# Performance work log

Hardware: AMD Instinct MI355X
Metric: run time of the kernel (lower is better)

## Reference

```python
import jax, jax.numpy as jnp
import numpy as np

B, N, D, H, L = 16, 1024, 256, 128, 2  # batch, nodes, feat dim, gcn_hidden, n_layers (D == 2*H)


def setup_inputs() -> dict:
    key = jax.random.key(0)
    ks = jax.random.split(key, 16)
    inp = {
        "gcn_input": jax.random.normal(ks[0], (B, N, D), jnp.float32),
        # scale adjacencies by 1/N so aggregated features stay O(1)
        "latent_adj": jax.random.uniform(ks[1], (B, N, N), jnp.float32) / N,
        "dep_adj": jax.random.uniform(ks[2], (B, N, N), jnp.float32) / N,
        # stacked per-layer parameters (leading dim L); layers share shapes since D == 2*H
        "refine_gate": jax.random.normal(ks[3], (L, D, 1), jnp.float32) * 0.02,
        "gate_W_in": jax.random.normal(ks[4], (L, D, 1), jnp.float32) * 0.02,
        "gate_b_in": jnp.zeros((L, 1), jnp.float32),
        "gate_W_out": jax.random.normal(ks[5], (L, D, 1), jnp.float32) * 0.02,
        "gate_b_out": jnp.zeros((L, 1), jnp.float32),
        "fc_in_W": jax.random.normal(ks[6], (L, H, D), jnp.float32) * 0.02,
        "fc_in_b": jnp.zeros((L, H), jnp.float32),
        "fc_out_W": jax.random.normal(ks[7], (L, H, D), jnp.float32) * 0.02,
        "fc_out_b": jnp.zeros((L, H), jnp.float32),
        "ln_g": jnp.ones((L, 2 * H), jnp.float32),
        "ln_b": jnp.zeros((L, 2 * H), jnp.float32),
    }
    return inp


def _gcn_layer(x, latent, dep, rg, Wgi, bgi, Wgo, bgo, Wi, bi, Wo, bo, g, b):
    # refine gate blends dependency and latent adjacency per source node
    gate = jax.nn.sigmoid(x @ rg)  # [B,N,1]
    A_in = gate * dep + (1.0 - gate) * latent  # [B,N,N]
    A_out = gate * jnp.swapaxes(dep, -1, -2) + (1.0 - gate) * jnp.swapaxes(latent, -1, -2)
    Ax_in = A_in @ x   # [B,N,D]
    Ax_out = A_out @ x
    # gcn gates (scalar bias added after the gated product, as in torch)
    Ax_in = Ax_in * jax.nn.sigmoid(Ax_in @ Wgi) + bgi
    Ax_out = Ax_out * jax.nn.sigmoid(Ax_out @ Wgo) + bgo
    # rec_fc(Ax) + rec_fc(x): weight applied to sum, bias counted twice (faithful)
    h_in = (Ax_in + x) @ Wi.T + 2.0 * bi   # [B,N,H]
    h_out = (Ax_out + x) @ Wo.T + 2.0 * bo
    h = jnp.concatenate([h_in, h_out], axis=-1)  # [B,N,2H]
    mu = jnp.mean(h, axis=-1, keepdims=True)
    var = jnp.var(h, axis=-1, keepdims=True)
    h = (h - mu) * jax.lax.rsqrt(var + 1e-5) * g + b
    return jax.nn.gelu(h, approximate=False)


def reference(gcn_input, latent_adj, dep_adj, refine_gate, gate_W_in, gate_b_in,
              gate_W_out, gate_b_out, fc_in_W, fc_in_b, fc_out_W, fc_out_b, ln_g, ln_b):
    x = gcn_input
    for l in range(refine_gate.shape[0]):  # small fixed layer count
        x = _gcn_layer(x, latent_adj, dep_adj, refine_gate[l],
                       gate_W_in[l], gate_b_in[l], gate_W_out[l], gate_b_out[l],
                       fc_in_W[l], fc_in_b[l], fc_out_W[l], fc_out_b[l],
                       ln_g[l], ln_b[l])
    return x
```

## Files before the change

### kernel.cpp

```cpp
#include <hip/hip_runtime.h>
#include <hip/hip_bf16.h>
#include <cstdint>

#define B_ 16
#define N_ 1024
#define D_ 256
#define H_ 128

typedef unsigned short u16;
typedef __attribute__((ext_vector_type(8))) short bf16x8;
typedef __attribute__((ext_vector_type(4))) float f32x4;

__device__ __forceinline__ u16 f2bf(float f) {
    union { float f; uint32_t u; } v; v.f = f;
    return (u16)((v.u + 0x7FFFu + ((v.u >> 16) & 1u)) >> 16);
}

typedef __attribute__((address_space(3))) void lds_void;
typedef const __attribute__((address_space(1))) void g_void;

__device__ __forceinline__ void gl_lds16(const void* g, void* l) {
    __builtin_amdgcn_global_load_lds((g_void*)g, (lds_void*)l, 16, 0, 0);
}

__device__ __forceinline__ void vm_wait5() { asm volatile("s_waitcnt vmcnt(5)" ::: "memory"); }
__device__ __forceinline__ void vm_wait0() { asm volatile("s_waitcnt vmcnt(0)" ::: "memory"); }

__global__ __launch_bounds__(256) void k_conv_adj(
    const float* __restrict__ dep, const float* __restrict__ lat,
    u16* __restrict__ depb, u16* __restrict__ latb,
    u16* __restrict__ depTb, u16* __restrict__ latTb)
{
    __shared__ u16 tile[64][64];
    const int bz = blockIdx.z;
    const int b = bz >> 1;
    const float* src = (bz & 1) ? lat : dep;
    u16* dstN = (bz & 1) ? latb : depb;
    u16* dstT = (bz & 1) ? latTb : depTb;
    const int r0 = blockIdx.y * 64, c0 = blockIdx.x * 64;
    const int t = threadIdx.x;
    const int r = t >> 2, cg = (t & 3) * 16;

    const float* srow = src + ((size_t)b * N_ + r0 + r) * N_ + c0 + cg;
    bf16x8 lo, hi;
    {
        const float4 v0 = *(const float4*)(srow);
        const float4 v1 = *(const float4*)(srow + 4);
        const float4 v2 = *(const float4*)(srow + 8);
        const float4 v3 = *(const float4*)(srow + 12);
        lo[0] = (short)f2bf(v0.x); lo[1] = (short)f2bf(v0.y); lo[2] = (short)f2bf(v0.z); lo[3] = (short)f2bf(v0.w);
        lo[4] = (short)f2bf(v1.x); lo[5] = (short)f2bf(v1.y); lo[6] = (short)f2bf(v1.z); lo[7] = (short)f2bf(v1.w);
        hi[0] = (short)f2bf(v2.x); hi[1] = (short)f2bf(v2.y); hi[2] = (short)f2bf(v2.z); hi[3] = (short)f2bf(v2.w);
        hi[4] = (short)f2bf(v3.x); hi[5] = (short)f2bf(v3.y); hi[6] = (short)f2bf(v3.z); hi[7] = (short)f2bf(v3.w);
    }
    u16* nrow = dstN + ((size_t)b * N_ + r0 + r) * N_ + c0 + cg;
    *(bf16x8*)nrow = lo;
    *(bf16x8*)(nrow + 8) = hi;

    const int g0 = (t & 3) * 2;
    const int s = r & 7;
    *(bf16x8*)(&tile[r][((g0    ) ^ s) * 8]) = lo;
    *(bf16x8*)(&tile[r][((g0 + 1) ^ s) * 8]) = hi;
    __syncthreads();

    const int sc = t >> 2, rg2 = (t & 3) * 16;
    bf16x8 o0, o1;
    #pragma unroll
    for (int i = 0; i < 8; ++i) {
        const int R = rg2 + i;
        o0[i] = (short)tile[R][(((sc >> 3) ^ (R & 7)) * 8) + (sc & 7)];
    }
    #pragma unroll
    for (int i = 0; i < 8; ++i) {
        const int R = rg2 + 8 + i;
        o1[i] = (short)tile[R][(((sc >> 3) ^ (R & 7)) * 8) + (sc & 7)];
    }
    u16* dT = dstT + ((size_t)b * N_ + c0 + sc) * N_ + r0 + rg2;
    *(bf16x8*)dT = o0;
    *(bf16x8*)(dT + 8) = o1;
}

__global__ __launch_bounds__(256) void k_gate_xt(
    const float* __restrict__ x, const float* __restrict__ rg,
    float* __restrict__ gate, u16* __restrict__ xT,
    const float* __restrict__ wi, const float* __restrict__ wo,
    u16* __restrict__ wib, u16* __restrict__ wob)
{
    if (blockIdx.y >= B_) {
        const int i = ((blockIdx.y - B_) * 32 + blockIdx.x) * 256 + threadIdx.x;
        wib[i] = f2bf(wi[i]);
        wob[i] = f2bf(wo[i]);
        return;
    }

    __shared__ u16 lx[D_][36];
    __shared__ float srg[D_];
    const int b = blockIdx.y, n0 = blockIdx.x * 32;
    const int t = threadIdx.x;
    srg[t] = rg[t];
    __syncthreads();

    const int r = t >> 3, cg = t & 7;
    const float* xrow = x + ((size_t)b * N_ + n0 + r) * D_;
    float dot = 0.f;
    #pragma unroll
    for (int u = 0; u < 8; ++u) {
        const int c = cg * 32 + u * 4;
        const float4 v = *(const float4*)(xrow + c);
        lx[c][r] = f2bf(v.x); lx[c + 1][r] = f2bf(v.y);
        lx[c + 2][r] = f2bf(v.z); lx[c + 3][r] = f2bf(v.w);
        dot += v.x * srg[c] + v.y * srg[c + 1] + v.z * srg[c + 2] + v.w * srg[c + 3];
    }
    dot += __shfl_down(dot, 4, 8);
    dot += __shfl_down(dot, 2, 8);
    dot += __shfl_down(dot, 1, 8);
    if (cg == 0) gate[(size_t)b * N_ + n0 + r] = 1.f / (1.f + expf(-dot));
    __syncthreads();

    #pragma unroll
    for (int i = 0; i < 8; ++i) {
        const int unit = i * 256 + t;
        const int d = unit >> 3, nch = (unit & 7) * 4;
        ushort4 wv;
        wv.x = lx[d][nch];     wv.y = lx[d][nch + 1];
        wv.z = lx[d][nch + 2]; wv.w = lx[d][nch + 3];
        *(ushort4*)(xT + ((size_t)b * D_ + d) * N_ + n0 + nch) = wv;
    }
}

__global__ __launch_bounds__(256, 2) void k_gemm_ax(
    const u16* __restrict__ depb, const u16* __restrict__ latb,
    const u16* __restrict__ depTb, const u16* __restrict__ latTb,
    const u16* __restrict__ xT,
    const float* __restrict__ gate,
    const float* __restrict__ Wgi, const float* __restrict__ Wgo,
    const float* __restrict__ bgi, const float* __restrict__ bgo,
    const float* __restrict__ xcur,
    u16* __restrict__ axin, u16* __restrict__ axout)
{
    __shared__ __align__(16) char smem[61696];
    float* hbuf = (float*)smem;
    float* sh_g = (float*)(smem + 61440);
    float* sh_s = (float*)(smem + 61568);

    const int bid = blockIdx.x;
    const int logical = (bid & 7) * 128 + (bid >> 3);
    const int b = logical >> 6;
    const int rem = logical & 63;
    const int z = rem >> 5;
    const int m0 = (rem & 31) * 32;

    const u16* A1 = z ? depTb : depb;
    const u16* A2 = z ? latTb : latb;
    const float* Wg = z ? Wgo : Wgi;
    const float bg0 = z ? bgo[0] : bgi[0];
    u16* outp = z ? axout : axin;

    const int t = threadIdx.x;
    const int lane = t & 63;
    const int w = t >> 6;

    f32x4 acc1[2][4], acc2[2][4];
    const f32x4 fz = {0.f, 0.f, 0.f, 0.f};
    #pragma unroll
    for (int i = 0; i < 2; ++i)
        #pragma unroll
        for (int j = 0; j < 4; ++j) { acc1[i][j] = fz; acc2[i][j] = fz; }

    const u16* gsrc[5];
    int loff[5];
    const int rl = lane >> 2;
    const int kk = (((lane & 3) ^ ((lane >> 3) & 3)) << 3);
    #pragma unroll
    for (int ci = 0; ci < 5; ++ci) {
        const int c = w * 5 + ci;
        if (c < 4) {
            const int cc = c & 1;
            const int m = cc * 16 + rl;
            const u16* base = (c < 2) ? A1 : A2;
            gsrc[ci] = base + ((size_t)b * N_ + m0 + m) * N_ + kk;
            loff[ci] = ((c < 2) ? 0 : 1024) + cc * 512;
        } else {
            const int cc = c - 4;
            const int n = cc * 16 + rl;
            gsrc[ci] = xT + ((size_t)b * D_ + n) * N_ + kk;
            loff[ci] = 2048 + cc * 512;
        }
    }

    u16* const sb = (u16*)smem;

    #pragma unroll
    for (int ci = 0; ci < 5; ++ci) gl_lds16(gsrc[ci], sb + loff[ci]);
    #pragma unroll
    for (int ci = 0; ci < 5; ++ci) { gl_lds16(gsrc[ci] + 32, sb + 10240 + loff[ci]); gsrc[ci] += 64; }

    const int mrow = lane & 15;
    const int kg = (((lane >> 4) ^ ((mrow >> 1) & 3)) << 3);

    for (int ks = 0; ks < N_ / 32; ++ks) {
        if (ks == 31) vm_wait0(); else vm_wait5();
        __builtin_amdgcn_s_barrier();
        __builtin_amdgcn_sched_barrier(0);
        if (ks <= 29) {
            u16* nb = sb + ((ks + 2) % 3) * 10240;
            #pragma unroll
            for (int ci = 0; ci < 5; ++ci) { gl_lds16(gsrc[ci], nb + loff[ci]); gsrc[ci] += 32; }
        }
        const u16* cur = sb + (ks % 3) * 10240;
        const u16* sA1 = cur;
        const u16* sA2 = cur + 1024;
        const u16* sB  = cur + 2048;
        bf16x8 a1[2], a2[2], fb[4];
        #pragma unroll
        for (int mt = 0; mt < 2; ++mt) {
            const int row = mt * 16 + mrow;
            a1[mt] = *(const bf16x8*)(sA1 + row * 32 + kg);
            a2[mt] = *(const bf16x8*)(sA2 + row * 32 + kg);
        }
        #pragma unroll
        for (int nt = 0; nt < 4; ++nt) {
            const int row = w * 64 + nt * 16 + mrow;
            fb[nt] = *(const bf16x8*)(sB + row * 32 + kg);
        }
        #pragma unroll
        for (int mt = 0; mt < 2; ++mt)
            #pragma unroll
            for (int nt = 0; nt < 4; ++nt) {
                acc1[mt][nt] = __builtin_amdgcn_mfma_f32_16x16x32_bf16(a1[mt], fb[nt], acc1[mt][nt], 0, 0, 0);
                acc2[mt][nt] = __builtin_amdgcn_mfma_f32_16x16x32_bf16(a2[mt], fb[nt], acc2[mt][nt], 0, 0, 0);
            }
    }
    __syncthreads();

    if (t < 32) sh_g[t] = gate[(size_t)b * N_ + m0 + t];
    __syncthreads();

    const int hi = lane >> 4;
    #pragma unroll
    for (int mt = 0; mt < 2; ++mt)
        #pragma unroll
        for (int nt = 0; nt < 4; ++nt) {
            const int col = w * 64 + nt * 16 + mrow;
            #pragma unroll
            for (int rr = 0; rr < 4; ++rr) {
                const int row = mt * 16 + hi * 4 + rr;
                const float g = sh_g[row];
                hbuf[row * 260 + col] = g * acc1[mt][nt][rr] + (1.f - g) * acc2[mt][nt][rr];
            }
        }
    __syncthreads();

    {
        const int rr = t >> 3;
        const int c0 = (t & 7) * 32;
        float dot = 0.f;
        #pragma unroll 8
        for (int u = 0; u < 32; ++u) dot += hbuf[rr * 260 + c0 + u] * Wg[c0 + u];
        dot += __shfl_down(dot, 4, 8);
        dot += __shfl_down(dot, 2, 8);
        dot += __shfl_down(dot, 1, 8);
        if ((t & 7) == 0) sh_s[rr] = 1.f / (1.f + expf(-dot));
    }
    __syncthreads();

    #pragma unroll
    for (int i = 0; i < 16; ++i) {
        const int row = (t >> 7) + i * 2;
        const int c = (t & 127) * 2;
        const float s = sh_s[row];
        const size_t gidx = ((size_t)b * N_ + m0 + row) * D_ + c;
        const float2 xv = *(const float2*)(xcur + gidx);
        const float v0 = hbuf[row * 260 + c] * s + bg0 + xv.x;
        const float v1 = hbuf[row * 260 + c + 1] * s + bg0 + xv.y;
        *(ushort2*)(outp + gidx) = make_ushort2(f2bf(v0), f2bf(v1));
    }
}

__global__ __launch_bounds__(256, 2) void k_fc_ln(
    const u16* __restrict__ axin, const u16* __restrict__ axout,
    const u16* __restrict__ Wib, const u16* __restrict__ Wob,
    const float* __restrict__ bi, const float* __restrict__ bo,
    const float* __restrict__ lg, const float* __restrict__ lb,
    float* __restrict__ outp)
{
    __shared__ __align__(16) char smem[61696];
    float* hbuf = (float*)smem;
    float* sh_mu = (float*)(smem + 61440);
    float* sh_rs = (float*)(smem + 61568);

    const int b = blockIdx.y, m0 = blockIdx.x * 32;
    const int t = threadIdx.x, lane = t & 63, w = t >> 6;
    const int half = w >> 1, wn = w & 1;

    f32x4 acc[2][4];
    const f32x4 fz = {0.f, 0.f, 0.f, 0.f};
    #pragma unroll
    for (int i = 0; i < 2; ++i)
        #pragma unroll
        for (int j = 0; j < 4; ++j) acc[i][j] = fz;

    const u16* gsrc[5];
    int loff[5];
    const int rl = lane >> 2;
    const int kk = (((lane & 3) ^ ((lane >> 3) & 3)) << 3);
    #pragma unroll
    for (int ci = 0; ci < 5; ++ci) {
        const int c = w * 5 + ci;
        if (c < 4) {
            const int cc = c & 1;
            const int m = cc * 16 + rl;
            const u16* base = (c < 2) ? axin : axout;
            gsrc[ci] = base + ((size_t)b * N_ + m0 + m) * D_ + kk;
            loff[ci] = ((c < 2) ? 0 : 1024) + cc * 512;
        } else {
            const int cc = (c - 4) & 7;
            const int n = cc * 16 + rl;
            const u16* base = (c < 12) ? Wib : Wob;
            gsrc[ci] = base + (size_t)n * D_ + kk;
            loff[ci] = ((c < 12) ? 2048 : 6144) + cc * 512;
        }
    }

    u16* const sb = (u16*)smem;

    #pragma unroll
    for (int ci = 0; ci < 5; ++ci) gl_lds16(gsrc[ci], sb + loff[ci]);
    #pragma unroll
    for (int ci = 0; ci < 5; ++ci) { gl_lds16(gsrc[ci] + 32, sb + 10240 + loff[ci]); gsrc[ci] += 64; }

    const int mrow = lane & 15;
    const int kg = (((lane >> 4) ^ ((mrow >> 1) & 3)) << 3);

    for (int ks = 0; ks < D_ / 32; ++ks) {
        if (ks == 7) vm_wait0(); else vm_wait5();
        __builtin_amdgcn_s_barrier();
        __builtin_amdgcn_sched_barrier(0);
        if (ks <= 5) {
            u16* nb = sb + ((ks + 2) % 3) * 10240;
            #pragma unroll
            for (int ci = 0; ci < 5; ++ci) { gl_lds16(gsrc[ci], nb + loff[ci]); gsrc[ci] += 32; }
        }
        const u16* cur = sb + (ks % 3) * 10240;
        const u16* sA = cur + (half ? 1024 : 0);
        const u16* sW = cur + 2048 + (half ? 4096 : 0);
        bf16x8 a[2], fb[4];
        #pragma unroll
        for (int mt = 0; mt < 2; ++mt)
            a[mt] = *(const bf16x8*)(sA + (mt * 16 + mrow) * 32 + kg);
        #pragma unroll
        for (int nt = 0; nt < 4; ++nt)
            fb[nt] = *(const bf16x8*)(sW + (wn * 64 + nt * 16 + mrow) * 32 + kg);
        #pragma unroll
        for (int mt = 0; mt < 2; ++mt)
            #pragma unroll
            for (int nt = 0; nt < 4; ++nt)
                acc[mt][nt] = __builtin_amdgcn_mfma_f32_16x16x32_bf16(a[mt], fb[nt], acc[mt][nt], 0, 0, 0);
    }
    __syncthreads();

    const int hi = lane >> 4;
    #pragma unroll
    for (int mt = 0; mt < 2; ++mt)
        #pragma unroll
        for (int nt = 0; nt < 4; ++nt) {
            const int colh = wn * 64 + nt * 16 + mrow;
            const int col = half * 128 + colh;
            const float bias = 2.f * (half ? bo[colh] : bi[colh]);
            #pragma unroll
            for (int rr = 0; rr < 4; ++rr) {
                const int row = mt * 16 + hi * 4 + rr;
                hbuf[row * 260 + col] = acc[mt][nt][rr] + bias;
            }
        }
    __syncthreads();

    {
        const int rr = t >> 3;
        const int c0 = (t & 7) * 32;
        float s = 0.f, ss = 0.f;
        #pragma unroll 8
        for (int u = 0; u < 32; ++u) {
            const float v = hbuf[rr * 260 + c0 + u];
            s += v; ss += v * v;
        }
        s += __shfl_down(s, 4, 8);  ss += __shfl_down(ss, 4, 8);
        s += __shfl_down(s, 2, 8);  ss += __shfl_down(ss, 2, 8);
        s += __shfl_down(s, 1, 8);  ss += __shfl_down(ss, 1, 8);
        if ((t & 7) == 0) {
            const float mu = s * (1.f / 256.f);
            const float var = ss * (1.f / 256.f) - mu * mu;
            sh_mu[rr] = mu;
            sh_rs[rr] = rsqrtf(var + 1e-5f);
        }
    }
    __syncthreads();

    #pragma unroll
    for (int i = 0; i < 16; ++i) {
        const int row = (t >> 7) + i * 2;
        const int c = (t & 127) * 2;
        const float mu = sh_mu[row], rs = sh_rs[row];
        const float2 gg = *(const float2*)(lg + c);
        const float2 bb = *(const float2*)(lb + c);
        const float v0 = (hbuf[row * 260 + c] - mu) * rs * gg.x + bb.x;
        const float v1 = (hbuf[row * 260 + c + 1] - mu) * rs * gg.y + bb.y;
        const float y0 = 0.5f * v0 * (1.f + erff(v0 * 0.70710678118654752f));
        const float y1 = 0.5f * v1 * (1.f + erff(v1 * 0.70710678118654752f));
        const size_t gidx = ((size_t)b * N_ + m0 + row) * D_ + c;
        *(float2*)(outp + gidx) = make_float2(y0, y1);
    }
}

extern "C" void kernel_launch(void* const* d_in, const int* in_sizes, int n_in,
                              void* d_out, int out_size, void* d_ws, size_t ws_size,
                              hipStream_t stream)
{
    (void)in_sizes; (void)n_in; (void)out_size; (void)ws_size;

    const float* x0  = (const float*)d_in[0];
    const float* lat = (const float*)d_in[1];
    const float* dep = (const float*)d_in[2];
    const float* rg  = (const float*)d_in[3];
    const float* Wgi = (const float*)d_in[4];
    const float* bgi = (const float*)d_in[5];
    const float* Wgo = (const float*)d_in[6];
    const float* bgo = (const float*)d_in[7];
    const float* fiW = (const float*)d_in[8];
    const float* fib = (const float*)d_in[9];
    const float* foW = (const float*)d_in[10];
    const float* fob = (const float*)d_in[11];
    const float* lng = (const float*)d_in[12];
    const float* lnb = (const float*)d_in[13];

    char* ws = (char*)d_ws;
    size_t off = 0;
    auto alloc = [&](size_t bytes) {
        char* p = ws + off;
        off += (bytes + 255) & ~(size_t)255;
        return p;
    };
    u16* depb  = (u16*)alloc(2ull * B_ * N_ * N_);
    u16* latb  = (u16*)alloc(2ull * B_ * N_ * N_);
    u16* depTb = (u16*)alloc(2ull * B_ * N_ * N_);
    u16* latTb = (u16*)alloc(2ull * B_ * N_ * N_);
    u16* xT    = (u16*)alloc(2ull * B_ * D_ * N_);
    u16* axin  = (u16*)alloc(2ull * B_ * N_ * D_);
    u16* axout = (u16*)alloc(2ull * B_ * N_ * D_);
    float* gate = (float*)alloc(4ull * B_ * N_);
    float* xbuf = (float*)alloc(4ull * B_ * N_ * D_);
    u16* Wib = (u16*)alloc(2ull * H_ * D_);
    u16* Wob = (u16*)alloc(2ull * H_ * D_);

    k_conv_adj<<<dim3(16, 16, 32), 256, 0, stream>>>(dep, lat, depb, latb, depTb, latTb);

    const float* xcur = x0;
    for (int l = 0; l < 2; ++l) {
        k_gate_xt<<<dim3(32, B_ + 4), 256, 0, stream>>>(
            xcur, rg + l * D_, gate, xT,
            fiW + (size_t)l * H_ * D_, foW + (size_t)l * H_ * D_, Wib, Wob);
        k_gemm_ax<<<dim3(1024), 256, 0, stream>>>(
            depb, latb, depTb, latTb, xT, gate,
            Wgi + l * D_, Wgo + l * D_, bgi + l, bgo + l,
            xcur, axin, axout);
        const bool last = (l == 1);
        k_fc_ln<<<dim3(32, B_), 256, 0, stream>>>(
            axin, axout, Wib, Wob,
            fib + l * H_, fob + l * H_,
            lng + l * 2 * H_, lnb + l * 2 * H_,
            last ? (float*)d_out : xbuf);
        xcur = xbuf;
    }
}
```

Measured before the change: 352.6 us.

## Blend adjacencies before the GEMM and enlarge aggregation tiles to 128 rows

```diff
diff --git a/kernel.cpp b/kernel.cpp
--- a/kernel.cpp
+++ b/kernel.cpp
@@ -15,6 +15,10 @@
     union { float f; uint32_t u; } v; v.f = f;
     return (u16)((v.u + 0x7FFFu + ((v.u >> 16) & 1u)) >> 16);
 }
+__device__ __forceinline__ float bf2f(u16 h) {
+    union { uint32_t u; float f; } v; v.u = ((uint32_t)h) << 16;
+    return v.f;
+}
 
 typedef __attribute__((address_space(3))) void lds_void;
 typedef const __attribute__((address_space(1))) void g_void;
@@ -23,8 +27,10 @@
     __builtin_amdgcn_global_load_lds((g_void*)g, (lds_void*)l, 16, 0, 0);
 }
 
-__device__ __forceinline__ void vm_wait5() { asm volatile("s_waitcnt vmcnt(5)" ::: "memory"); }
+__device__ __forceinline__ void vm_wait4() { asm volatile("s_waitcnt vmcnt(4)" ::: "memory"); }
+__device__ __forceinline__ void vm_wait2() { asm volatile("s_waitcnt vmcnt(2)" ::: "memory"); }
 __device__ __forceinline__ void vm_wait0() { asm volatile("s_waitcnt vmcnt(0)" ::: "memory"); }
+__device__ __forceinline__ void lgkm0()   { asm volatile("s_waitcnt lgkmcnt(0)" ::: "memory"); }
 
 __global__ __launch_bounds__(256) void k_conv_adj(
     const float* __restrict__ dep, const float* __restrict__ lat,
@@ -128,7 +134,7 @@
     }
 }
 
-__global__ __launch_bounds__(256, 2) void k_gemm_ax(
+__global__ __launch_bounds__(512, 2) void k_gemm_ax(
     const u16* __restrict__ depb, const u16* __restrict__ latb,
     const u16* __restrict__ depTb, const u16* __restrict__ latTb,
     const u16* __restrict__ xT,
@@ -138,17 +144,18 @@
     const float* __restrict__ xcur,
     u16* __restrict__ axin, u16* __restrict__ axout)
 {
-    __shared__ __align__(16) char smem[61696];
+    __shared__ __align__(16) char smem[51712];
+    u16* const sb = (u16*)smem;
     float* hbuf = (float*)smem;
-    float* sh_g = (float*)(smem + 61440);
-    float* sh_s = (float*)(smem + 61568);
+    float* psum = (float*)(smem + 49152);
+    float* sh_s = (float*)(smem + 51200);
 
     const int bid = blockIdx.x;
-    const int logical = (bid & 7) * 128 + (bid >> 3);
-    const int b = logical >> 6;
-    const int rem = logical & 63;
-    const int z = rem >> 5;
-    const int m0 = (rem & 31) * 32;
+    const int logical = (bid & 7) * 32 + (bid >> 3);
+    const int b = logical >> 4;
+    const int rem = logical & 15;
+    const int z = rem >> 3;
+    const int m0 = (rem & 7) * 128;
 
     const u16* A1 = z ? depTb : depb;
     const u16* A2 = z ? latTb : latb;
@@ -159,121 +166,162 @@
     const int t = threadIdx.x;
     const int lane = t & 63;
     const int w = t >> 6;
-
-    f32x4 acc1[2][4], acc2[2][4];
-    const f32x4 fz = {0.f, 0.f, 0.f, 0.f};
-    #pragma unroll
-    for (int i = 0; i < 2; ++i)
-        #pragma unroll
-        for (int j = 0; j < 4; ++j) { acc1[i][j] = fz; acc2[i][j] = fz; }
-
-    const u16* gsrc[5];
-    int loff[5];
+    const int wr = w >> 2, wc = w & 3;
+
+    const int arow = t >> 2;
+    const int akq = t & 3;
+    const float gv = gate[(size_t)b * N_ + m0 + arow];
+    const u16* gA1 = A1 + ((size_t)b * N_ + m0 + arow) * N_ + akq * 8;
+    const u16* gA2 = A2 + ((size_t)b * N_ + m0 + arow) * N_ + akq * 8;
+    const int awoff = arow * 32 + ((akq ^ ((arow >> 1) & 3)) << 3);
+
     const int rl = lane >> 2;
     const int kk = (((lane & 3) ^ ((lane >> 3) & 3)) << 3);
-    #pragma unroll
-    for (int ci = 0; ci < 5; ++ci) {
-        const int c = w * 5 + ci;
-        if (c < 4) {
-            const int cc = c & 1;
-            const int m = cc * 16 + rl;
-            const u16* base = (c < 2) ? A1 : A2;
-            gsrc[ci] = base + ((size_t)b * N_ + m0 + m) * N_ + kk;
-            loff[ci] = ((c < 2) ? 0 : 1024) + cc * 512;
-        } else {
-            const int cc = c - 4;
-            const int n = cc * 16 + rl;
-            gsrc[ci] = xT + ((size_t)b * D_ + n) * N_ + kk;
-            loff[ci] = 2048 + cc * 512;
-        }
-    }
-
-    u16* const sb = (u16*)smem;
-
-    #pragma unroll
-    for (int ci = 0; ci < 5; ++ci) gl_lds16(gsrc[ci], sb + loff[ci]);
-    #pragma unroll
-    for (int ci = 0; ci < 5; ++ci) { gl_lds16(gsrc[ci] + 32, sb + 10240 + loff[ci]); gsrc[ci] += 64; }
+    const u16* gB0 = xT + ((size_t)b * D_ + (w * 2) * 16 + rl) * N_ + kk;
+    const u16* gB1 = xT + ((size_t)b * D_ + (w * 2 + 1) * 16 + rl) * N_ + kk;
+    const int boff0 = 4096 + (w * 2) * 512;
+    const int boff1 = 4096 + (w * 2 + 1) * 512;
 
     const int mrow = lane & 15;
+    const int hi = lane >> 4;
     const int kg = (((lane >> 4) ^ ((mrow >> 1) & 3)) << 3);
 
-    for (int ks = 0; ks < N_ / 32; ++ks) {
-        if (ks == 31) vm_wait0(); else vm_wait5();
+    f32x4 acc[4][4];
+    const f32x4 fz = {0.f, 0.f, 0.f, 0.f};
+    #pragma unroll
+    for (int i = 0; i < 4; ++i)
+        #pragma unroll
+        for (int j = 0; j < 4; ++j) acc[i][j] = fz;
+
+    bf16x8 rA1x, rA2x, rA1y, rA2y;
+
+    auto blend_store = [&](const bf16x8& a1v, const bf16x8& a2v, u16* dst) {
+        bf16x8 bl;
+        #pragma unroll
+        for (int u = 0; u < 8; ++u) {
+            const float f1 = bf2f((u16)a1v[u]);
+            const float f2 = bf2f((u16)a2v[u]);
+            bl[u] = (short)f2bf(f2 + gv * (f1 - f2));
+        }
+        *(bf16x8*)dst = bl;
+    };
+
+    rA1x = *(const bf16x8*)(gA1);       rA2x = *(const bf16x8*)(gA2);
+    blend_store(rA1x, rA2x, sb + awoff);
+    rA1x = *(const bf16x8*)(gA1 + 32);  rA2x = *(const bf16x8*)(gA2 + 32);
+    gl_lds16(gB0, sb + boff0);          gl_lds16(gB1, sb + boff1);
+    blend_store(rA1x, rA2x, sb + 12288 + awoff);
+    rA1x = *(const bf16x8*)(gA1 + 64);  rA2x = *(const bf16x8*)(gA2 + 64);
+    gl_lds16(gB0 + 32, sb + 12288 + boff0); gl_lds16(gB1 + 32, sb + 12288 + boff1);
+    vm_wait4();
+    lgkm0();
+    __builtin_amdgcn_sched_barrier(0);
+    __builtin_amdgcn_s_barrier();
+    __builtin_amdgcn_sched_barrier(0);
+
+    auto body = [&](int ks, bf16x8& c1, bf16x8& c2, bf16x8& n1, bf16x8& n2) {
+        if (ks <= 28) {
+            n1 = *(const bf16x8*)(gA1 + (ks + 3) * 32);
+            n2 = *(const bf16x8*)(gA2 + (ks + 3) * 32);
+        }
+        const u16* sA = sb + (ks & 1) * 12288;
+        const u16* sBc = sA + 4096;
+        bf16x8 a[4], fbv[4];
+        #pragma unroll
+        for (int mt = 0; mt < 4; ++mt)
+            a[mt] = *(const bf16x8*)(sA + (wr * 64 + mt * 16 + mrow) * 32 + kg);
+        #pragma unroll
+        for (int nt = 0; nt < 4; ++nt)
+            fbv[nt] = *(const bf16x8*)(sBc + (wc * 64 + nt * 16 + mrow) * 32 + kg);
+        #pragma unroll
+        for (int mt = 0; mt < 4; ++mt)
+            #pragma unroll
+            for (int nt = 0; nt < 4; ++nt)
+                acc[mt][nt] = __builtin_amdgcn_mfma_f32_16x16x32_bf16(a[mt], fbv[nt], acc[mt][nt], 0, 0, 0);
+        __builtin_amdgcn_sched_barrier(0);
         __builtin_amdgcn_s_barrier();
         __builtin_amdgcn_sched_barrier(0);
         if (ks <= 29) {
-            u16* nb = sb + ((ks + 2) % 3) * 10240;
-            #pragma unroll
-            for (int ci = 0; ci < 5; ++ci) { gl_lds16(gsrc[ci], nb + loff[ci]); gsrc[ci] += 32; }
-        }
-        const u16* cur = sb + (ks % 3) * 10240;
-        const u16* sA1 = cur;
-        const u16* sA2 = cur + 1024;
-        const u16* sB  = cur + 2048;
-        bf16x8 a1[2], a2[2], fb[4];
-        #pragma unroll
-        for (int mt = 0; mt < 2; ++mt) {
-            const int row = mt * 16 + mrow;
-            a1[mt] = *(const bf16x8*)(sA1 + row * 32 + kg);
-            a2[mt] = *(const bf16x8*)(sA2 + row * 32 + kg);
-        }
-        #pragma unroll
-        for (int nt = 0; nt < 4; ++nt) {
-            const int row = w * 64 + nt * 16 + mrow;
-            fb[nt] = *(const bf16x8*)(sB + row * 32 + kg);
-        }
-        #pragma unroll
-        for (int mt = 0; mt < 2; ++mt)
-            #pragma unroll
-            for (int nt = 0; nt < 4; ++nt) {
-                acc1[mt][nt] = __builtin_amdgcn_mfma_f32_16x16x32_bf16(a1[mt], fb[nt], acc1[mt][nt], 0, 0, 0);
-                acc2[mt][nt] = __builtin_amdgcn_mfma_f32_16x16x32_bf16(a2[mt], fb[nt], acc2[mt][nt], 0, 0, 0);
+            u16* cb = sb + (ks & 1) * 12288;
+            blend_store(c1, c2, cb + awoff);
+            gl_lds16(gB0 + (ks + 2) * 32, cb + boff0);
+            gl_lds16(gB1 + (ks + 2) * 32, cb + boff1);
+        }
+        if (ks <= 28) vm_wait4();
+        else if (ks == 29) vm_wait2();
+        else if (ks == 30) vm_wait0();
+        lgkm0();
+        __builtin_amdgcn_sched_barrier(0);
+        __builtin_amdgcn_s_barrier();
+        __builtin_amdgcn_sched_barrier(0);
+    };
+
+    for (int kp = 0; kp < 16; ++kp) {
+        body(2 * kp,     rA1x, rA2x, rA1y, rA2y);
+        body(2 * kp + 1, rA1y, rA2y, rA1x, rA2x);
+    }
+    __syncthreads();
+
+    float wgv[4];
+    #pragma unroll
+    for (int nt = 0; nt < 4; ++nt) wgv[nt] = Wg[wc * 64 + nt * 16 + mrow];
+    #pragma unroll
+    for (int mt = 0; mt < 4; ++mt) {
+        #pragma unroll
+        for (int rr = 0; rr < 4; ++rr) {
+            float p = acc[mt][0][rr] * wgv[0] + acc[mt][1][rr] * wgv[1]
+                    + acc[mt][2][rr] * wgv[2] + acc[mt][3][rr] * wgv[3];
+            p += __shfl_xor(p, 1, 16);
+            p += __shfl_xor(p, 2, 16);
+            p += __shfl_xor(p, 4, 16);
+            p += __shfl_xor(p, 8, 16);
+            if (mrow == 0) psum[(wr * 64 + mt * 16 + hi * 4 + rr) * 4 + wc] = p;
+        }
+    }
+    __syncthreads();
+    if (t < 128) {
+        const float d = psum[t * 4] + psum[t * 4 + 1] + psum[t * 4 + 2] + psum[t * 4 + 3];
+        sh_s[t] = 1.f / (1.f + expf(-d));
+    }
+    __syncthreads();
+
+    #pragma unroll
+    for (int p = 0; p < 4; ++p) {
+        if (wr == (p >> 1)) {
+            #pragma unroll
+            for (int mtl = 0; mtl < 2; ++mtl) {
+                const int mt = (p & 1) * 2 + mtl;
+                #pragma unroll
+                for (int nt = 0; nt < 4; ++nt) {
+                    const int col = wc * 64 + nt * 16 + mrow;
+                    #pragma unroll
+                    for (int rr = 0; rr < 4; ++rr) {
+                        const int hrow = mtl * 16 + hi * 4 + rr;
+                        hbuf[hrow * 260 + col] = acc[mt][nt][rr];
+                    }
+                }
             }
-    }
-    __syncthreads();
-
-    if (t < 32) sh_g[t] = gate[(size_t)b * N_ + m0 + t];
-    __syncthreads();
-
-    const int hi = lane >> 4;
-    #pragma unroll
-    for (int mt = 0; mt < 2; ++mt)
-        #pragma unroll
-        for (int nt = 0; nt < 4; ++nt) {
-            const int col = w * 64 + nt * 16 + mrow;
-            #pragma unroll
-            for (int rr = 0; rr < 4; ++rr) {
-                const int row = mt * 16 + hi * 4 + rr;
-                const float g = sh_g[row];
-                hbuf[row * 260 + col] = g * acc1[mt][nt][rr] + (1.f - g) * acc2[mt][nt][rr];
-            }
-        }
-    __syncthreads();
-
-    {
-        const int rr = t >> 3;
-        const int c0 = (t & 7) * 32;
-        float dot = 0.f;
-        #pragma unroll 8
-        for (int u = 0; u < 32; ++u) dot += hbuf[rr * 260 + c0 + u] * Wg[c0 + u];
-        dot += __shfl_down(dot, 4, 8);
-        dot += __shfl_down(dot, 2, 8);
-        dot += __shfl_down(dot, 1, 8);
-        if ((t & 7) == 0) sh_s[rr] = 1.f / (1.f + expf(-dot));
-    }
-    __syncthreads();
-
-    #pragma unroll
-    for (int i = 0; i < 16; ++i) {
-        const int row = (t >> 7) + i * 2;
-        const int c = (t & 127) * 2;
-        const float s = sh_s[row];
-        const size_t gidx = ((size_t)b * N_ + m0 + row) * D_ + c;
-        const float2 xv = *(const float2*)(xcur + gidx);
-        const float v0 = hbuf[row * 260 + c] * s + bg0 + xv.x;
-        const float v1 = hbuf[row * 260 + c + 1] * s + bg0 + xv.y;
-        *(ushort2*)(outp + gidx) = make_ushort2(f2bf(v0), f2bf(v1));
+        }
+        __syncthreads();
+        {
+            const int sr = t >> 4;
+            const int sc0 = (t & 15) * 16;
+            const int grow = p * 32 + sr;
+            const float s = sh_s[grow];
+            const size_t gb = ((size_t)b * N_ + m0 + grow) * D_ + sc0;
+            const float* xr = xcur + gb;
+            u16* orow = outp + gb;
+            bf16x8 o0, o1;
+            #pragma unroll
+            for (int u = 0; u < 8; ++u)
+                o0[u] = (short)f2bf(hbuf[sr * 260 + sc0 + u] * s + bg0 + xr[u]);
+            #pragma unroll
+            for (int u = 0; u < 8; ++u)
+                o1[u] = (short)f2bf(hbuf[sr * 260 + sc0 + 8 + u] * s + bg0 + xr[8 + u]);
+            *(bf16x8*)orow = o0;
+            *(bf16x8*)(orow + 8) = o1;
+        }
+        __syncthreads();
     }
 }
 
@@ -333,7 +381,7 @@
     const int kg = (((lane >> 4) ^ ((mrow >> 1) & 3)) << 3);
 
     for (int ks = 0; ks < D_ / 32; ++ks) {
-        if (ks == 7) vm_wait0(); else vm_wait5();
+        if (ks == 7) vm_wait0(); else { asm volatile("s_waitcnt vmcnt(5)" ::: "memory"); }
         __builtin_amdgcn_s_barrier();
         __builtin_amdgcn_sched_barrier(0);
         if (ks <= 5) {
@@ -459,7 +507,7 @@
         k_gate_xt<<<dim3(32, B_ + 4), 256, 0, stream>>>(
             xcur, rg + l * D_, gate, xT,
             fiW + (size_t)l * H_ * D_, foW + (size_t)l * H_ * D_, Wib, Wob);
-        k_gemm_ax<<<dim3(1024), 256, 0, stream>>>(
+        k_gemm_ax<<<dim3(256), 512, 0, stream>>>(
             depb, latb, depTb, latTb, xT, gate,
             Wgi + l * D_, Wgo + l * D_, bgi + l, bgo + l,
             xcur, axin, axout);
```

Measured after the change: 321.0 us. 9.0% less time.
